# Optimization experiments

Hardware: AMD Instinct MI355X
Metric: run time of the kernel (lower is better)

## Reference

```python
import jax, jax.numpy as jnp
import numpy as np

B, S, E, H = 8, 2048, 512, 8
D = E // H  # head_dim = 64


def setup_inputs() -> dict:
    key0 = jax.random.key(0)
    ks = jax.random.split(key0, 12)
    scale = 1.0 / np.sqrt(E)
    return {
        "value": jax.random.normal(ks[0], (B, S, E), jnp.float32),
        "key": jax.random.normal(ks[1], (B, S, E), jnp.float32),
        "query": jax.random.normal(ks[2], (B, S, E), jnp.float32),
        "mask": jax.random.randint(ks[3], (B, 1, 1, S), 0, 2, jnp.int32),
        "wq": jax.random.normal(ks[4], (E, E), jnp.float32) * scale,
        "bq": jnp.zeros((E,), jnp.float32),
        "wk": jax.random.normal(ks[5], (E, E), jnp.float32) * scale,
        "bk": jnp.zeros((E,), jnp.float32),
        "wv": jax.random.normal(ks[6], (E, E), jnp.float32) * scale,
        "bv": jnp.zeros((E,), jnp.float32),
        "wo": jax.random.normal(ks[7], (E, E), jnp.float32) * scale,
        "bo": jnp.zeros((E,), jnp.float32),
    }


def reference(value, key, query, mask, wq, bq, wk, bk, wv, bv, wo, bo):
    b, s, e = query.shape
    # projections
    q = (query @ wq + bq).reshape(b, s, H, D)  # (B,S,H,D)
    k = (key @ wk + bk).reshape(b, s, H, D)
    v = (value @ wv + bv).reshape(b, s, H, D)
    # scaled dot-product logits: (B,H,Sq,Sk)
    logits = jnp.einsum("bqhd,bkhd->bhqk", q, k) / jnp.sqrt(jnp.asarray(D, q.dtype))
    logits = logits + mask.astype(logits.dtype) * -1e9  # mask==1 -> blocked
    attn = jax.nn.softmax(logits, axis=-1)
    out = jnp.einsum("bhqk,bkhd->bqhd", attn, v).reshape(b, s, e)
    return out @ wo + bo
```

## Files before the change

kernel.cpp:

```cpp
#include <hip/hip_runtime.h>

#define Bz 8
#define Sz 2048
#define Ez 512
#define Hz 8
#define Dz 64

typedef _Float16 f16;
typedef __attribute__((ext_vector_type(2))) _Float16 f16x2;
typedef __attribute__((ext_vector_type(8))) _Float16 f16x8;
typedef __attribute__((ext_vector_type(4))) float f32x4;

#define LOG2E 1.44269504f

__device__ __forceinline__ void async16(const void* g, void* l) {
    __builtin_amdgcn_global_load_lds(
        (const __attribute__((address_space(1))) unsigned int*)g,
        (__attribute__((address_space(3))) unsigned int*)l, 16, 0, 0);
}

__device__ __forceinline__ f16x2 pkrtz(float a, float b) {
    return __builtin_bit_cast(f16x2, __builtin_amdgcn_cvt_pkrtz(a, b));
}

__global__ __launch_bounds__(256)
void cast_kernel(const float* __restrict__ q, const float* __restrict__ k,
                 const float* __restrict__ v, const int* __restrict__ msk,
                 f16* __restrict__ qa, f16* __restrict__ ka,
                 f16* __restrict__ va, float* __restrict__ mf)
{
    const int z = blockIdx.y;
    const int idx = blockIdx.x * 256 + threadIdx.x;
    if (z < 3) {
        const float* src = (z == 0) ? q : (z == 1) ? k : v;
        f16* dst = (z == 0) ? qa : (z == 1) ? ka : va;
        float4 x = *(const float4*)&src[(size_t)idx * 4];
        f16x2 h0 = pkrtz(x.x, x.y), h1 = pkrtz(x.z, x.w);
        f16 h[4] = {h0[0], h0[1], h1[0], h1[1]};
        *(uint2*)&dst[(size_t)idx * 4] = *(uint2*)h;
    } else {
        if (idx < Bz * Sz) mf[idx] = msk[idx] ? -1.0e9f : (-6.0f * LOG2E);
    }
}

__global__ __launch_bounds__(256)
void prep_w(const float* __restrict__ W0, const float* __restrict__ W1,
            const float* __restrict__ W2, const float* __restrict__ W3,
            f16* __restrict__ T0, f16* __restrict__ T1,
            f16* __restrict__ T2, f16* __restrict__ T3)
{
    __shared__ float S[64][68];
    const float* W = (blockIdx.z==0)?W0:(blockIdx.z==1)?W1:(blockIdx.z==2)?W2:W3;
    f16*         T = (blockIdx.z==0)?T0:(blockIdx.z==1)?T1:(blockIdx.z==2)?T2:T3;
    const float sc = (blockIdx.z == 0) ? 0.125f * LOG2E : 1.0f;
    const int k0 = blockIdx.x * 64, n0 = blockIdx.y * 64;
    const int tid = threadIdx.x;
    {
        int kr = tid >> 4, nc = (tid & 15) * 4;
        #pragma unroll
        for (int i = 0; i < 4; ++i) {
            float4 w4 = *(const float4*)&W[(size_t)(k0 + kr + i*16) * Ez + n0 + nc];
            S[kr + i*16][nc+0] = w4.x; S[kr + i*16][nc+1] = w4.y;
            S[kr + i*16][nc+2] = w4.z; S[kr + i*16][nc+3] = w4.w;
        }
    }
    __syncthreads();
    {
        int n = tid >> 2, kq = tid & 3;
        f16 h[16];
        #pragma unroll
        for (int j = 0; j < 16; ++j) h[j] = (f16)(S[kq*16 + j][n] * sc);
        f16* dst = &T[(size_t)(n0 + n) * Ez + k0 + kq*16];
        *(uint4*)&dst[0] = *(uint4*)&h[0];
        *(uint4*)&dst[8] = *(uint4*)&h[8];
    }
}

#define TRSTR 136

__global__ __launch_bounds__(256, 4)
void proj_gemm(const f16* __restrict__ qa, const f16* __restrict__ ka,
               const f16* __restrict__ va,
               const f16* __restrict__ wtq, const f16* __restrict__ wtk,
               const f16* __restrict__ wtv,
               const float* __restrict__ bqp, const float* __restrict__ bkp,
               const float* __restrict__ bvp,
               f16* __restrict__ qp, f16* __restrict__ kp, f16* __restrict__ vp)
{
    __shared__ __align__(16) char lds[34816];
    const int z = blockIdx.z;
    const f16* A  = (z==0)?qa:(z==1)?ka:va;
    const f16* Wt = (z==0)?wtq:(z==1)?wtk:wtv;
    const float* bias = (z==0)?bqp:(z==1)?bkp:bvp;
    f16* C16 = (z==0)?qp:(z==1)?kp:vp;
    const float bscale = (z==0) ? 0.125f*LOG2E : 1.0f;
    const int mode = (z==2) ? 2 : 1;

    const int tid  = threadIdx.x;
    const int lane = tid & 63, w = tid >> 6;
    const int col  = lane & 15, quad = lane >> 4;
    const int wm = w & 1, wn = w >> 1;
    const int m0 = blockIdx.x * 128, n0 = blockIdx.y * 128;
    const int srow = lane >> 2, schunk = lane & 3;

    f32x4 acc[4][4];
    #pragma unroll
    for (int i = 0; i < 4; ++i)
        #pragma unroll
        for (int j = 0; j < 4; ++j) acc[i][j] = (f32x4){0.f,0.f,0.f,0.f};

    auto issue = [&](int t, int buf) {
        f16* As = (f16*)(lds + buf * 16384);
        f16* Ws = As + 4096;
        #pragma unroll
        for (int i = 0; i < 2; ++i) {
            int row = w*32 + i*16 + srow;
            int cl = schunk ^ ((row >> 1) & 3);
            async16(&A[(size_t)(m0 + row) * Ez + t*32 + cl*8],  &As[row*32 + schunk*8]);
            async16(&Wt[(size_t)(n0 + row) * Ez + t*32 + cl*8], &Ws[row*32 + schunk*8]);
        }
    };

    issue(0, 0);
    const int xrc = (col >> 1) & 3;

    for (int t = 0; t < 16; ++t) {
        const int cur = t & 1;
        __syncthreads();
        if (t < 15) issue(t + 1, cur ^ 1);
        f16* As = (f16*)(lds + cur * 16384);
        f16* Ws = As + 4096;
        f16x8 af[4];
        #pragma unroll
        for (int mi = 0; mi < 4; ++mi)
            af[mi] = *(const f16x8*)&As[(wm*64 + mi*16 + col)*32 + ((quad ^ xrc)*8)];
        #pragma unroll
        for (int ni = 0; ni < 4; ++ni) {
            f16x8 wf = *(const f16x8*)&Ws[(wn*64 + ni*16 + col)*32 + ((quad ^ xrc)*8)];
            #pragma unroll
            for (int mi = 0; mi < 4; ++mi)
                acc[mi][ni] = __builtin_amdgcn_mfma_f32_16x16x32_f16(af[mi], wf, acc[mi][ni], 0,0,0);
        }
    }

    f16* Tr = (f16*)lds;
    __syncthreads();
    #pragma unroll
    for (int ni = 0; ni < 4; ++ni) {
        int nl = wn*64 + ni*16 + col;
        float bv = bias[n0 + nl] * bscale;
        #pragma unroll
        for (int mi = 0; mi < 4; ++mi)
            #pragma unroll
            for (int rr = 0; rr < 4; ++rr) {
                int ml = wm*64 + mi*16 + quad*4 + rr;
                f16 v = (f16)(acc[mi][ni][rr] + bv);
                if (mode == 1) Tr[ml*TRSTR + nl] = v;
                else           Tr[nl*TRSTR + ml] = v;
            }
    }
    __syncthreads();
    const int rw = tid >> 1, half = tid & 1;
    const f16* srcp = &Tr[rw*TRSTR + half*64];
    if (mode == 1) {
        int m = m0 + rw, b = m >> 11, s = m & (Sz-1);
        int hh = (n0 >> 6) + half;
        f16* dst = &C16[(((size_t)b*Hz + hh)*Sz + s)*Dz];
        #pragma unroll
        for (int j = 0; j < 8; ++j)
            *(uint4*)&dst[j*8] = *(const uint4*)&srcp[j*8];
    } else {
        int n = n0 + rw, hh = n >> 6, d = n & 63;
        int b = m0 >> 11, sbase = (m0 & (Sz-1)) + half*64;
        f16* dst = &C16[(((size_t)b*Hz + hh)*Dz + d)*Sz + sbase];
        #pragma unroll
        for (int j = 0; j < 8; ++j)
            *(uint4*)&dst[j*8] = *(const uint4*)&srcp[j*8];
    }
}

__global__ __launch_bounds__(256, 4)
void out_gemm(const f16* __restrict__ A, const f16* __restrict__ Wt,
              const float* __restrict__ bias, float* __restrict__ Cf)
{
    __shared__ __align__(16) char lds[32768];
    const int tid  = threadIdx.x;
    const int lane = tid & 63, w = tid >> 6;
    const int col  = lane & 15, quad = lane >> 4;
    const int wm = w & 1, wn = w >> 1;
    const int m0 = blockIdx.x * 128, n0 = blockIdx.y * 128;
    const int srow = lane >> 2, schunk = lane & 3;

    f32x4 acc[4][4];
    #pragma unroll
    for (int i = 0; i < 4; ++i)
        #pragma unroll
        for (int j = 0; j < 4; ++j) acc[i][j] = (f32x4){0.f,0.f,0.f,0.f};

    auto issue = [&](int t, int buf) {
        f16* As = (f16*)(lds + buf * 16384);
        f16* Ws = As + 4096;
        #pragma unroll
        for (int i = 0; i < 2; ++i) {
            int row = w*32 + i*16 + srow;
            int cl = schunk ^ ((row >> 1) & 3);
            async16(&A[(size_t)(m0 + row) * Ez + t*32 + cl*8],  &As[row*32 + schunk*8]);
            async16(&Wt[(size_t)(n0 + row) * Ez + t*32 + cl*8], &Ws[row*32 + schunk*8]);
        }
    };

    issue(0, 0);
    const int xrc = (col >> 1) & 3;

    for (int t = 0; t < 16; ++t) {
        const int cur = t & 1;
        __syncthreads();
        if (t < 15) issue(t + 1, cur ^ 1);
        f16* As = (f16*)(lds + cur * 16384);
        f16* Ws = As + 4096;
        f16x8 af[4];
        #pragma unroll
        for (int mi = 0; mi < 4; ++mi)
            af[mi] = *(const f16x8*)&As[(wm*64 + mi*16 + col)*32 + ((quad ^ xrc)*8)];
        #pragma unroll
        for (int ni = 0; ni < 4; ++ni) {
            f16x8 wf = *(const f16x8*)&Ws[(wn*64 + ni*16 + col)*32 + ((quad ^ xrc)*8)];
            #pragma unroll
            for (int mi = 0; mi < 4; ++mi)
                acc[mi][ni] = __builtin_amdgcn_mfma_f32_16x16x32_f16(af[mi], wf, acc[mi][ni], 0,0,0);
        }
    }

    #pragma unroll
    for (int ni = 0; ni < 4; ++ni) {
        int n = n0 + wn*64 + ni*16 + col;
        float bv = bias[n];
        #pragma unroll
        for (int mi = 0; mi < 4; ++mi)
            #pragma unroll
            for (int rr = 0; rr < 4; ++rr) {
                int m = m0 + wm*64 + mi*16 + quad*4 + rr;
                Cf[(size_t)m * Ez + n] = acc[mi][ni][rr] + bv;
            }
    }
}

__global__ __launch_bounds__(256, 4)
void attn_f16(const f16* __restrict__ Q, const f16* __restrict__ K,
              const f16* __restrict__ VT, const float* __restrict__ MF,
              f16* __restrict__ O)
{
    __shared__ __align__(16) f16 KS[2][64*64];
    __shared__ __align__(16) f16 VS[2][64*64];

    const int tid  = threadIdx.x;
    const int lane = tid & 63, w = tid >> 6;
    const int col  = lane & 15, quad = lane >> 4;

    const int blk = blockIdx.x;
    const int xcd = blk & 7, slot = blk >> 3;
    const int bh = xcd + 8 * (slot >> 4);
    const int qb = slot & 15;
    const int b = bh >> 3, h = bh & 7;

    const int q0 = qb * 128 + w * 32;

    f16x8 qf[2][2];
    #pragma unroll
    for (int qt = 0; qt < 2; ++qt)
        #pragma unroll
        for (int ks = 0; ks < 2; ++ks)
            qf[qt][ks] = *(const f16x8*)&Q[((size_t)bh*Sz + q0 + qt*16 + col)*Dz + ks*32 + quad*8];

    const f16* Kp = K + (size_t)bh * Sz * Dz;
    const f16* Vp = VT + (size_t)bh * Dz * Sz;
    const float* mp = MF + (size_t)b * Sz;

    const int srow = lane >> 3, sch = lane & 7;

    int keyrow[4], gk[4];
    #pragma unroll
    for (int kc = 0; kc < 4; ++kc) {
        keyrow[kc] = 32*(kc>>1) + 8*(col>>2) + 4*(kc&1) + (col&3);
        gk[kc] = (keyrow[kc] & 7) ^ ((2*((keyrow[kc] >> 3) & 3)) & 7);
    }

    f32x4 oacc[2][4];
    #pragma unroll
    for (int qt = 0; qt < 2; ++qt)
        #pragma unroll
        for (int dc = 0; dc < 4; ++dc) oacc[qt][dc] = (f32x4){0.f,0.f,0.f,0.f};
    float lsum[2] = {0.f, 0.f};

    auto issue = [&](int t, int buf) {
        #pragma unroll
        for (int i = 0; i < 2; ++i) {
            int row = w*16 + i*8 + srow;
            int g = (row & 7) ^ ((2*((row >> 3) & 3)) & 7);
            int cl = sch ^ g;
            async16(&Kp[((size_t)t*64 + row)*Dz + cl*8], &KS[buf][row*64 + sch*8]);
            async16(&Vp[(size_t)row*Sz + t*64 + cl*8],   &VS[buf][row*64 + sch*8]);
        }
    };

    issue(0, 0);

    for (int t = 0; t < 32; ++t) {
        const int cur = t & 1;
        __syncthreads();
        if (t < 31) issue(t + 1, cur ^ 1);

        f32x4 sc[2][4];
        #pragma unroll
        for (int kc = 0; kc < 4; ++kc) {
            f32x4 mk = *(const f32x4*)&mp[t*64 + 32*(kc>>1) + 4*(kc&1) + 8*quad];
            sc[0][kc] = mk;
            sc[1][kc] = mk;
        }
        #pragma unroll
        for (int kc = 0; kc < 4; ++kc) {
            #pragma unroll
            for (int ks = 0; ks < 2; ++ks) {
                f16x8 kf = *(const f16x8*)&KS[cur][keyrow[kc]*64 + (((ks*4 + quad) ^ gk[kc])*8)];
                sc[0][kc] = __builtin_amdgcn_mfma_f32_16x16x32_f16(kf, qf[0][ks], sc[0][kc], 0,0,0);
                sc[1][kc] = __builtin_amdgcn_mfma_f32_16x16x32_f16(kf, qf[1][ks], sc[1][kc], 0,0,0);
            }
        }

        union { f16x2 h2[4]; f16x8 h8; } ph[2][2];
        #pragma unroll
        for (int qt = 0; qt < 2; ++qt) {
            #pragma unroll
            for (int kg = 0; kg < 2; ++kg) {
                float e0 = exp2f(sc[qt][2*kg][0]), e1 = exp2f(sc[qt][2*kg][1]);
                float e2 = exp2f(sc[qt][2*kg][2]), e3 = exp2f(sc[qt][2*kg][3]);
                float e4 = exp2f(sc[qt][2*kg+1][0]), e5 = exp2f(sc[qt][2*kg+1][1]);
                float e6 = exp2f(sc[qt][2*kg+1][2]), e7 = exp2f(sc[qt][2*kg+1][3]);
                lsum[qt] += ((e0+e1)+(e2+e3)) + ((e4+e5)+(e6+e7));
                ph[qt][kg].h2[0] = pkrtz(e0, e1);
                ph[qt][kg].h2[1] = pkrtz(e2, e3);
                ph[qt][kg].h2[2] = pkrtz(e4, e5);
                ph[qt][kg].h2[3] = pkrtz(e6, e7);
            }
        }

        #pragma unroll
        for (int dc = 0; dc < 4; ++dc) {
            const int d = dc*16 + col;
            const int gd = (d & 7) ^ ((2*((d >> 3) & 3)) & 7);
            #pragma unroll
            for (int kg = 0; kg < 2; ++kg) {
                f16x8 vf = *(const f16x8*)&VS[cur][d*64 + (((kg*4 + quad) ^ gd)*8)];
                oacc[0][dc] = __builtin_amdgcn_mfma_f32_16x16x32_f16(vf, ph[0][kg].h8, oacc[0][dc], 0,0,0);
                oacc[1][dc] = __builtin_amdgcn_mfma_f32_16x16x32_f16(vf, ph[1][kg].h8, oacc[1][dc], 0,0,0);
            }
        }
    }

    float inv[2];
    #pragma unroll
    for (int qt = 0; qt < 2; ++qt) {
        float v = lsum[qt];
        v += __shfl_xor(v, 16, 64);
        v += __shfl_xor(v, 32, 64);
        inv[qt] = 1.0f / v;
    }
    #pragma unroll
    for (int qt = 0; qt < 2; ++qt) {
        const int q = q0 + qt*16 + col;
        f16* op = &O[((size_t)b*Sz + q)*Ez + h*Dz];
        #pragma unroll
        for (int dc = 0; dc < 4; ++dc) {
            f16 ov[4] = {(f16)(oacc[qt][dc][0]*inv[qt]), (f16)(oacc[qt][dc][1]*inv[qt]),
                         (f16)(oacc[qt][dc][2]*inv[qt]), (f16)(oacc[qt][dc][3]*inv[qt])};
            *(uint2*)&op[dc*16 + quad*4] = *(uint2*)ov;
        }
    }
}

extern "C" void kernel_launch(void* const* d_in, const int* in_sizes, int n_in,
                              void* d_out, int out_size, void* d_ws, size_t ws_size,
                              hipStream_t stream)
{
    const float* value = (const float*)d_in[0];
    const float* key   = (const float*)d_in[1];
    const float* query = (const float*)d_in[2];
    const int*   mask  = (const int*)d_in[3];
    const float* wq = (const float*)d_in[4];
    const float* bq = (const float*)d_in[5];
    const float* wk = (const float*)d_in[6];
    const float* bk = (const float*)d_in[7];
    const float* wv = (const float*)d_in[8];
    const float* bv = (const float*)d_in[9];
    const float* wo = (const float*)d_in[10];
    const float* bo = (const float*)d_in[11];
    float* out = (float*)d_out;

    const size_t nW   = (size_t)Ez * Ez;
    const size_t nAct = (size_t)Bz * Sz * Ez;
    f16* wtq = (f16*)d_ws;
    f16* wtk = wtq + nW;
    f16* wtv = wtk + nW;
    f16* wto = wtv + nW;
    f16* qa  = wto + nW;
    f16* ka  = qa + nAct;
    f16* va  = ka + nAct;
    f16* qp  = va + nAct;
    f16* kp  = qp + nAct;
    f16* vp  = kp + nAct;
    f16* o16 = vp + nAct;
    float* mskf = (float*)(o16 + nAct);

    cast_kernel<<<dim3(8192, 4), 256, 0, stream>>>(query, key, value, mask, qa, ka, va, mskf);
    prep_w<<<dim3(8, 8, 4), 256, 0, stream>>>(wq, wk, wv, wo, wtq, wtk, wtv, wto);

    proj_gemm<<<dim3(128, 4, 3), 256, 0, stream>>>(qa, ka, va, wtq, wtk, wtv,
                                                   bq, bk, bv, qp, kp, vp);

    attn_f16<<<1024, 256, 0, stream>>>(qp, kp, vp, mskf, o16);

    out_gemm<<<dim3(128, 4), 256, 0, stream>>>(o16, wto, bo, out);
}
```

Before: 334.1 us.

## Skip masked keys by compacting unmasked key indices per batch

A new kernel builds a per-batch prefix-sum list of unmasked key positions and their count. A second new kernel gathers and transposes the matching V rows into a compact buffer. Attention then gathers K rows through that index list and loops only over tiles of unmasked keys, zeroing the softmax sum for padding in the last tile; this replaces the additive mask, whose blocked keys contributed nothing. The projection and output GEMMs also drop LDS double buffering to use less LDS, and the projection epilogue writes V in row layout. The cost is two extra launches and an extra V pass, and the GEMMs can no longer overlap loads with compute.

```diff
diff --git a/kernel.cpp b/kernel.cpp
--- a/kernel.cpp
+++ b/kernel.cpp
@@ -23,24 +23,23 @@
     return __builtin_bit_cast(f16x2, __builtin_amdgcn_cvt_pkrtz(a, b));
 }
 
+__device__ __forceinline__ int swz(int row) {
+    return (row & 7) ^ ((2 * ((row >> 3) & 3)) & 7);
+}
+
 __global__ __launch_bounds__(256)
 void cast_kernel(const float* __restrict__ q, const float* __restrict__ k,
-                 const float* __restrict__ v, const int* __restrict__ msk,
-                 f16* __restrict__ qa, f16* __restrict__ ka,
-                 f16* __restrict__ va, float* __restrict__ mf)
+                 const float* __restrict__ v,
+                 f16* __restrict__ qa, f16* __restrict__ ka, f16* __restrict__ va)
 {
     const int z = blockIdx.y;
     const int idx = blockIdx.x * 256 + threadIdx.x;
-    if (z < 3) {
-        const float* src = (z == 0) ? q : (z == 1) ? k : v;
-        f16* dst = (z == 0) ? qa : (z == 1) ? ka : va;
-        float4 x = *(const float4*)&src[(size_t)idx * 4];
-        f16x2 h0 = pkrtz(x.x, x.y), h1 = pkrtz(x.z, x.w);
-        f16 h[4] = {h0[0], h0[1], h1[0], h1[1]};
-        *(uint2*)&dst[(size_t)idx * 4] = *(uint2*)h;
-    } else {
-        if (idx < Bz * Sz) mf[idx] = msk[idx] ? -1.0e9f : (-6.0f * LOG2E);
-    }
+    const float* src = (z == 0) ? q : (z == 1) ? k : v;
+    f16* dst = (z == 0) ? qa : (z == 1) ? ka : va;
+    float4 x = *(const float4*)&src[(size_t)idx * 4];
+    f16x2 h0 = pkrtz(x.x, x.y), h1 = pkrtz(x.z, x.w);
+    f16 h[4] = {h0[0], h0[1], h1[0], h1[1]};
+    *(uint2*)&dst[(size_t)idx * 4] = *(uint2*)h;
 }
 
 __global__ __launch_bounds__(256)
@@ -76,7 +75,73 @@
     }
 }
 
-#define TRSTR 136
+__global__ __launch_bounds__(256)
+void mask_index(const int* __restrict__ mask, int* __restrict__ idx,
+                int* __restrict__ slen)
+{
+    __shared__ int sc2[2][256];
+    __shared__ int stot;
+    const int b = blockIdx.x, tid = threadIdx.x;
+    const int* mp = mask + (size_t)b * Sz;
+    int m[8], c = 0;
+    #pragma unroll
+    for (int j = 0; j < 8; ++j) { m[j] = mp[tid*8 + j]; c += (m[j] == 0); }
+    sc2[0][tid] = c;
+    __syncthreads();
+    int src = 0;
+    #pragma unroll
+    for (int s = 1; s < 256; s <<= 1) {
+        int v = sc2[src][tid] + ((tid >= s) ? sc2[src][tid - s] : 0);
+        sc2[src ^ 1][tid] = v;
+        src ^= 1;
+        __syncthreads();
+    }
+    int incl = sc2[src][tid];
+    int base = incl - c;
+    if (tid == 255) { slen[b] = incl; stot = incl; }
+    int k = base;
+    #pragma unroll
+    for (int j = 0; j < 8; ++j)
+        if (m[j] == 0) idx[(size_t)b * Sz + (k++)] = tid*8 + j;
+    __syncthreads();
+    for (int j = stot + tid; j < Sz; j += 256) idx[(size_t)b * Sz + j] = 0;
+}
+
+__global__ __launch_bounds__(256)
+void compact_v(const f16* __restrict__ vp, const int* __restrict__ idx,
+               const int* __restrict__ slen, f16* __restrict__ vt)
+{
+    const int ct = blockIdx.x, h = blockIdx.y, b = blockIdx.z;
+    const int sl = slen[b];
+    if (ct * 64 >= sl) {
+        if (ct > 0 || sl > 0) return;
+    }
+    __shared__ f16 S[64 * 72];
+    const int tid = threadIdx.x;
+    {
+        int r = tid >> 2, ch = tid & 3;
+        int j = ct * 64 + r;
+        uint4 v0 = {0,0,0,0}, v1 = {0,0,0,0};
+        if (j < sl) {
+            int s = idx[(size_t)b * Sz + j];
+            const f16* srcp = vp + (((size_t)b * Hz + h) * Sz + s) * Dz + ch * 16;
+            v0 = *(const uint4*)&srcp[0];
+            v1 = *(const uint4*)&srcp[8];
+        }
+        *(uint4*)&S[r*72 + ch*16]     = v0;
+        *(uint4*)&S[r*72 + ch*16 + 8] = v1;
+    }
+    __syncthreads();
+    {
+        int d = tid >> 2, kq = tid & 3;
+        f16 hh[16];
+        #pragma unroll
+        for (int j = 0; j < 16; ++j) hh[j] = S[(kq*16 + j)*72 + d];
+        f16* dst = vt + (((size_t)b * Hz + h) * Dz + d) * Sz + ct*64 + kq*16;
+        *(uint4*)&dst[0] = *(uint4*)&hh[0];
+        *(uint4*)&dst[8] = *(uint4*)&hh[8];
+    }
+}
 
 __global__ __launch_bounds__(256, 4)
 void proj_gemm(const f16* __restrict__ qa, const f16* __restrict__ ka,
@@ -87,14 +152,13 @@
                const float* __restrict__ bvp,
                f16* __restrict__ qp, f16* __restrict__ kp, f16* __restrict__ vp)
 {
-    __shared__ __align__(16) char lds[34816];
+    __shared__ __align__(16) char lds[18432];
     const int z = blockIdx.z;
     const f16* A  = (z==0)?qa:(z==1)?ka:va;
     const f16* Wt = (z==0)?wtq:(z==1)?wtk:wtv;
     const float* bias = (z==0)?bqp:(z==1)?bkp:bvp;
     f16* C16 = (z==0)?qp:(z==1)?kp:vp;
     const float bscale = (z==0) ? 0.125f*LOG2E : 1.0f;
-    const int mode = (z==2) ? 2 : 1;
 
     const int tid  = threadIdx.x;
     const int lane = tid & 63, w = tid >> 6;
@@ -103,15 +167,19 @@
     const int m0 = blockIdx.x * 128, n0 = blockIdx.y * 128;
     const int srow = lane >> 2, schunk = lane & 3;
 
+    f16* As = (f16*)lds;
+    f16* Ws = As + 4096;
+
     f32x4 acc[4][4];
     #pragma unroll
     for (int i = 0; i < 4; ++i)
         #pragma unroll
         for (int j = 0; j < 4; ++j) acc[i][j] = (f32x4){0.f,0.f,0.f,0.f};
 
-    auto issue = [&](int t, int buf) {
-        f16* As = (f16*)(lds + buf * 16384);
-        f16* Ws = As + 4096;
+    const int xrc = (col >> 1) & 3;
+
+    for (int t = 0; t < 16; ++t) {
+        __syncthreads();
         #pragma unroll
         for (int i = 0; i < 2; ++i) {
             int row = w*32 + i*16 + srow;
@@ -119,17 +187,7 @@
             async16(&A[(size_t)(m0 + row) * Ez + t*32 + cl*8],  &As[row*32 + schunk*8]);
             async16(&Wt[(size_t)(n0 + row) * Ez + t*32 + cl*8], &Ws[row*32 + schunk*8]);
         }
-    };
-
-    issue(0, 0);
-    const int xrc = (col >> 1) & 3;
-
-    for (int t = 0; t < 16; ++t) {
-        const int cur = t & 1;
-        __syncthreads();
-        if (t < 15) issue(t + 1, cur ^ 1);
-        f16* As = (f16*)(lds + cur * 16384);
-        f16* Ws = As + 4096;
+        __syncthreads();
         f16x8 af[4];
         #pragma unroll
         for (int mi = 0; mi < 4; ++mi)
@@ -144,37 +202,30 @@
     }
 
     f16* Tr = (f16*)lds;
-    __syncthreads();
-    #pragma unroll
-    for (int ni = 0; ni < 4; ++ni) {
-        int nl = wn*64 + ni*16 + col;
-        float bv = bias[n0 + nl] * bscale;
-        #pragma unroll
-        for (int mi = 0; mi < 4; ++mi)
-            #pragma unroll
-            for (int rr = 0; rr < 4; ++rr) {
-                int ml = wm*64 + mi*16 + quad*4 + rr;
-                f16 v = (f16)(acc[mi][ni][rr] + bv);
-                if (mode == 1) Tr[ml*TRSTR + nl] = v;
-                else           Tr[nl*TRSTR + ml] = v;
-            }
-    }
-    __syncthreads();
-    const int rw = tid >> 1, half = tid & 1;
-    const f16* srcp = &Tr[rw*TRSTR + half*64];
-    if (mode == 1) {
+    #pragma unroll
+    for (int p = 0; p < 2; ++p) {
+        __syncthreads();
+        if (wn == p) {
+            #pragma unroll
+            for (int ni = 0; ni < 4; ++ni) {
+                float bv = bias[n0 + p*64 + ni*16 + col] * bscale;
+                #pragma unroll
+                for (int mi = 0; mi < 4; ++mi)
+                    #pragma unroll
+                    for (int rr = 0; rr < 4; ++rr) {
+                        int ml = wm*64 + mi*16 + quad*4 + rr;
+                        Tr[ml*72 + ni*16 + col] = (f16)(acc[mi][ni][rr] + bv);
+                    }
+            }
+        }
+        __syncthreads();
+        int rw = tid >> 1, half = tid & 1;
         int m = m0 + rw, b = m >> 11, s = m & (Sz-1);
-        int hh = (n0 >> 6) + half;
-        f16* dst = &C16[(((size_t)b*Hz + hh)*Sz + s)*Dz];
-        #pragma unroll
-        for (int j = 0; j < 8; ++j)
-            *(uint4*)&dst[j*8] = *(const uint4*)&srcp[j*8];
-    } else {
-        int n = n0 + rw, hh = n >> 6, d = n & 63;
-        int b = m0 >> 11, sbase = (m0 & (Sz-1)) + half*64;
-        f16* dst = &C16[(((size_t)b*Hz + hh)*Dz + d)*Sz + sbase];
-        #pragma unroll
-        for (int j = 0; j < 8; ++j)
+        int hh = (n0 >> 6) + p;
+        f16* dst = &C16[(((size_t)b*Hz + hh)*Sz + s)*Dz + half*32];
+        const f16* srcp = &Tr[rw*72 + half*32];
+        #pragma unroll
+        for (int j = 0; j < 4; ++j)
             *(uint4*)&dst[j*8] = *(const uint4*)&srcp[j*8];
     }
 }
@@ -183,7 +234,7 @@
 void out_gemm(const f16* __restrict__ A, const f16* __restrict__ Wt,
               const float* __restrict__ bias, float* __restrict__ Cf)
 {
-    __shared__ __align__(16) char lds[32768];
+    __shared__ __align__(16) char lds[16384];
     const int tid  = threadIdx.x;
     const int lane = tid & 63, w = tid >> 6;
     const int col  = lane & 15, quad = lane >> 4;
@@ -191,15 +242,19 @@
     const int m0 = blockIdx.x * 128, n0 = blockIdx.y * 128;
     const int srow = lane >> 2, schunk = lane & 3;
 
+    f16* As = (f16*)lds;
+    f16* Ws = As + 4096;
+
     f32x4 acc[4][4];
     #pragma unroll
     for (int i = 0; i < 4; ++i)
         #pragma unroll
         for (int j = 0; j < 4; ++j) acc[i][j] = (f32x4){0.f,0.f,0.f,0.f};
 
-    auto issue = [&](int t, int buf) {
-        f16* As = (f16*)(lds + buf * 16384);
-        f16* Ws = As + 4096;
+    const int xrc = (col >> 1) & 3;
+
+    for (int t = 0; t < 16; ++t) {
+        __syncthreads();
         #pragma unroll
         for (int i = 0; i < 2; ++i) {
             int row = w*32 + i*16 + srow;
@@ -207,17 +262,7 @@
             async16(&A[(size_t)(m0 + row) * Ez + t*32 + cl*8],  &As[row*32 + schunk*8]);
             async16(&Wt[(size_t)(n0 + row) * Ez + t*32 + cl*8], &Ws[row*32 + schunk*8]);
         }
-    };
-
-    issue(0, 0);
-    const int xrc = (col >> 1) & 3;
-
-    for (int t = 0; t < 16; ++t) {
-        const int cur = t & 1;
-        __syncthreads();
-        if (t < 15) issue(t + 1, cur ^ 1);
-        f16* As = (f16*)(lds + cur * 16384);
-        f16* Ws = As + 4096;
+        __syncthreads();
         f16x8 af[4];
         #pragma unroll
         for (int mi = 0; mi < 4; ++mi)
@@ -247,8 +292,8 @@
 
 __global__ __launch_bounds__(256, 4)
 void attn_f16(const f16* __restrict__ Q, const f16* __restrict__ K,
-              const f16* __restrict__ VT, const float* __restrict__ MF,
-              f16* __restrict__ O)
+              const f16* __restrict__ VT, const int* __restrict__ idx,
+              const int* __restrict__ slen, f16* __restrict__ O)
 {
     __shared__ __align__(16) f16 KS[2][64*64];
     __shared__ __align__(16) f16 VS[2][64*64];
@@ -263,6 +308,9 @@
     const int qb = slot & 15;
     const int b = bh >> 3, h = bh & 7;
 
+    const int sl = slen[b];
+    const int nt = (sl + 63) >> 6;
+
     const int q0 = qb * 128 + w * 32;
 
     f16x8 qf[2][2];
@@ -274,15 +322,18 @@
 
     const f16* Kp = K + (size_t)bh * Sz * Dz;
     const f16* Vp = VT + (size_t)bh * Dz * Sz;
-    const float* mp = MF + (size_t)b * Sz;
+    const int* ixp = idx + (size_t)b * Sz;
 
     const int srow = lane >> 3, sch = lane & 7;
+    const int row0 = w*16 + srow, row1 = row0 + 8;
+    const int g0 = swz(row0), g1 = swz(row1);
+    const int cl0 = sch ^ g0, cl1 = sch ^ g1;
 
     int keyrow[4], gk[4];
     #pragma unroll
     for (int kc = 0; kc < 4; ++kc) {
         keyrow[kc] = 32*(kc>>1) + 8*(col>>2) + 4*(kc&1) + (col&3);
-        gk[kc] = (keyrow[kc] & 7) ^ ((2*((keyrow[kc] >> 3) & 3)) & 7);
+        gk[kc] = swz(keyrow[kc]);
     }
 
     f32x4 oacc[2][4];
@@ -292,31 +343,34 @@
         for (int dc = 0; dc < 4; ++dc) oacc[qt][dc] = (f32x4){0.f,0.f,0.f,0.f};
     float lsum[2] = {0.f, 0.f};
 
-    auto issue = [&](int t, int buf) {
-        #pragma unroll
-        for (int i = 0; i < 2; ++i) {
-            int row = w*16 + i*8 + srow;
-            int g = (row & 7) ^ ((2*((row >> 3) & 3)) & 7);
-            int cl = sch ^ g;
-            async16(&Kp[((size_t)t*64 + row)*Dz + cl*8], &KS[buf][row*64 + sch*8]);
-            async16(&Vp[(size_t)row*Sz + t*64 + cl*8],   &VS[buf][row*64 + sch*8]);
-        }
+    auto issue = [&](int t, int buf, int s0, int s1) {
+        async16(&Kp[(size_t)s0*Dz + cl0*8],          &KS[buf][row0*64 + sch*8]);
+        async16(&Vp[(size_t)row0*Sz + t*64 + cl0*8], &VS[buf][row0*64 + sch*8]);
+        async16(&Kp[(size_t)s1*Dz + cl1*8],          &KS[buf][row1*64 + sch*8]);
+        async16(&Vp[(size_t)row1*Sz + t*64 + cl1*8], &VS[buf][row1*64 + sch*8]);
     };
 
-    issue(0, 0);
-
-    for (int t = 0; t < 32; ++t) {
+    int cs0 = ixp[row0], cs1 = ixp[row1];
+    issue(0, 0, cs0, cs1);
+    int ns0 = 0, ns1 = 0;
+    if (nt > 1) { ns0 = ixp[64 + row0]; ns1 = ixp[64 + row1]; }
+
+    for (int t = 0; t < nt; ++t) {
         const int cur = t & 1;
         __syncthreads();
-        if (t < 31) issue(t + 1, cur ^ 1);
+        if (t + 1 < nt) {
+            issue(t + 1, cur ^ 1, ns0, ns1);
+            if (t + 2 < nt) {
+                ns0 = ixp[(t+2)*64 + row0];
+                ns1 = ixp[(t+2)*64 + row1];
+            }
+        }
 
         f32x4 sc[2][4];
         #pragma unroll
-        for (int kc = 0; kc < 4; ++kc) {
-            f32x4 mk = *(const f32x4*)&mp[t*64 + 32*(kc>>1) + 4*(kc&1) + 8*quad];
-            sc[0][kc] = mk;
-            sc[1][kc] = mk;
-        }
+        for (int qt = 0; qt < 2; ++qt)
+            #pragma unroll
+            for (int kc = 0; kc < 4; ++kc) sc[qt][kc] = (f32x4){0.f,0.f,0.f,0.f};
         #pragma unroll
         for (int kc = 0; kc < 4; ++kc) {
             #pragma unroll
@@ -327,6 +381,7 @@
             }
         }
 
+        const bool last = (t == nt - 1);
         union { f16x2 h2[4]; f16x8 h8; } ph[2][2];
         #pragma unroll
         for (int qt = 0; qt < 2; ++qt) {
@@ -336,7 +391,17 @@
                 float e2 = exp2f(sc[qt][2*kg][2]), e3 = exp2f(sc[qt][2*kg][3]);
                 float e4 = exp2f(sc[qt][2*kg+1][0]), e5 = exp2f(sc[qt][2*kg+1][1]);
                 float e6 = exp2f(sc[qt][2*kg+1][2]), e7 = exp2f(sc[qt][2*kg+1][3]);
-                lsum[qt] += ((e0+e1)+(e2+e3)) + ((e4+e5)+(e6+e7));
+                float ls;
+                if (last) {
+                    int rem = sl - t*64 - 32*kg - 8*quad;
+                    ls = ((rem > 0 ? e0 : 0.f) + (rem > 1 ? e1 : 0.f))
+                       + ((rem > 2 ? e2 : 0.f) + (rem > 3 ? e3 : 0.f))
+                       + ((rem > 4 ? e4 : 0.f) + (rem > 5 ? e5 : 0.f))
+                       + ((rem > 6 ? e6 : 0.f) + (rem > 7 ? e7 : 0.f));
+                } else {
+                    ls = ((e0 + e1) + (e2 + e3)) + ((e4 + e5) + (e6 + e7));
+                }
+                lsum[qt] += ls;
                 ph[qt][kg].h2[0] = pkrtz(e0, e1);
                 ph[qt][kg].h2[1] = pkrtz(e2, e3);
                 ph[qt][kg].h2[2] = pkrtz(e4, e5);
@@ -347,7 +412,7 @@
         #pragma unroll
         for (int dc = 0; dc < 4; ++dc) {
             const int d = dc*16 + col;
-            const int gd = (d & 7) ^ ((2*((d >> 3) & 3)) & 7);
+            const int gd = swz(d);
             #pragma unroll
             for (int kg = 0; kg < 2; ++kg) {
                 f16x8 vf = *(const f16x8*)&VS[cur][d*64 + (((kg*4 + quad) ^ gd)*8)];
@@ -408,16 +473,21 @@
     f16* qp  = va + nAct;
     f16* kp  = qp + nAct;
     f16* vp  = kp + nAct;
-    f16* o16 = vp + nAct;
-    float* mskf = (float*)(o16 + nAct);
-
-    cast_kernel<<<dim3(8192, 4), 256, 0, stream>>>(query, key, value, mask, qa, ka, va, mskf);
+    f16* vt  = vp + nAct;
+    f16* o16 = vt + nAct;
+    int* idxp = (int*)(o16 + nAct);
+    int* slenp = idxp + Bz * Sz;
+
+    cast_kernel<<<dim3(8192, 3), 256, 0, stream>>>(query, key, value, qa, ka, va);
     prep_w<<<dim3(8, 8, 4), 256, 0, stream>>>(wq, wk, wv, wo, wtq, wtk, wtv, wto);
+    mask_index<<<Bz, 256, 0, stream>>>(mask, idxp, slenp);
 
     proj_gemm<<<dim3(128, 4, 3), 256, 0, stream>>>(qa, ka, va, wtq, wtk, wtv,
                                                    bq, bk, bv, qp, kp, vp);
 
-    attn_f16<<<1024, 256, 0, stream>>>(qp, kp, vp, mskf, o16);
+    compact_v<<<dim3(32, Hz, Bz), 256, 0, stream>>>(vp, idxp, slenp, vt);
+
+    attn_f16<<<1024, 256, 0, stream>>>(qp, kp, vt, idxp, slenp, o16);
 
     out_gemm<<<dim3(128, 4), 256, 0, stream>>>(o16, wto, bo, out);
 }
```

Measured after the change: 300.5 us. -10.0%, faster.
